# Kernel optimization log

Hardware: AMD Instinct MI355X
Metric: run time of the kernel (lower is better)

Reference implementation:

```python
import jax, jax.numpy as jnp
import numpy as np

N = 50000   # nodes
E = 800000  # raw (non-self-loop) edges
H = 4       # attention heads


def _att_coef(h, src, dst, mask, n):
    # per-edge cosine similarity (sklearn cosine_similarity gathered at edges)
    hn = h / jnp.maximum(jnp.linalg.norm(h, axis=-1, keepdims=True), 1e-12)
    sim = jnp.sum(hn[src] * hn[dst], axis=-1)              # [E]
    # threshold sim<0.1 -> 0; mask keeps only edges surviving previous layers
    sim = jnp.where(mask & (sim >= 0.1), sim, 0.0)
    # l1 row-normalization (rows indexed by src, matching adj.row)
    rowsum = jax.ops.segment_sum(sim, src, num_segments=n)
    safe = jnp.where(rowsum[src] > 0, rowsum[src], 1.0)
    att = jnp.where(rowsum[src] > 0, sim / safe, 0.0)
    new_mask = att > 0                                     # nonzero structure after threshold
    degree = jax.ops.segment_sum(new_mask.astype(h.dtype), src, num_segments=n)
    lam = 1.0 / (degree + 1.0)                             # self-loop weight per node
    att_w = jnp.where(new_mask, jnp.exp(att), 0.0)         # exp() of surviving entries
    self_w = jnp.exp(lam)
    return att_w, self_w, new_mask


def _gat_layer(h, W, a, b, src, dst, n, act):
    # DGL GATConv: W projection, additive attention, softmax over incoming edges
    HF = W.shape[1]
    F = HF // H
    feat = (h @ W).reshape(n, H, F)                        # [N,H,F]
    el = jnp.sum(feat * a[0], axis=-1)                     # [N,H]
    er = jnp.sum(feat * a[1], axis=-1)                     # [N,H]
    e = jax.nn.leaky_relu(el[src] + er[dst], 0.2)          # [Eg,H]
    emax = jax.ops.segment_max(e, dst, num_segments=n)
    ex = jnp.exp(e - emax[dst])
    z = jax.ops.segment_sum(ex, dst, num_segments=n)
    alpha = ex / z[dst]                                    # edge softmax over dst
    out = jax.ops.segment_sum(feat[src] * alpha[..., None], dst, num_segments=n)
    out = out.reshape(n, HF) + b
    return jax.nn.leaky_relu(out, 0.01) if act else out


def setup_inputs() -> dict:
    key = jax.random.key(0)
    ks = jax.random.split(key, 9)
    x = jax.random.normal(ks[0], (N, 128), jnp.float32)
    src = jax.random.randint(ks[1], (E,), 0, N, jnp.int32)
    dst = jax.random.randint(ks[2], (E,), 0, N, jnp.int32)
    dst = jnp.where(dst == src, (dst + 1) % N, dst)  # raw edges have no self-loops
    W0 = jax.random.normal(ks[3], (128, H * 64), jnp.float32) * 0.05
    a0 = jax.random.normal(ks[4], (2, H, 64), jnp.float32) * 0.05
    b0 = jnp.zeros((H * 64,), jnp.float32)
    W1 = jax.random.normal(ks[5], (H * 64, H * 64), jnp.float32) * 0.05
    a1 = jax.random.normal(ks[6], (2, H, 64), jnp.float32) * 0.05
    b1 = jnp.zeros((H * 64,), jnp.float32)
    return {"x": x, "edge_src": src, "edge_dst": dst,
            "W0": W0, "a0": a0, "b0": b0, "W1": W1, "a1": a1, "b1": b1}


def reference(x, edge_src, edge_dst, W0, a0, b0, W1, a1, b1):
    sl = jnp.arange(N, dtype=edge_src.dtype)
    src_g = jnp.concatenate([edge_src, sl])  # GATConv graph includes self-loops
    dst_g = jnp.concatenate([edge_dst, sl])
    mask = jnp.ones((E,), bool)
    # layer 0: att_coef on input features, then GATConv (+ leaky_relu activation)
    att_w, self_w, mask = _att_coef(x, edge_src, edge_dst, mask, N)
    h = _gat_layer(x, W0, a0, b0, src_g, dst_g, N, True)
    # layer 1: att_coef on hidden features (edge set shrunk by layer-0 threshold)
    att_w, self_w, mask = _att_coef(h, edge_src, edge_dst, mask, N)
    h = _gat_layer(h, W1, a1, b1, src_g, dst_g, N, False)
    return h, att_w, self_w
```

## Files before the change

### kernel.cpp

```cpp
#include <hip/hip_runtime.h>


#define NH 4
#define NF 64
#define HF 256

__device__ __forceinline__ float wred_sum(float v) {
#pragma unroll
  for (int o = 32; o > 0; o >>= 1) v += __shfl_xor(v, o, 64);
  return v;
}
__device__ __forceinline__ float lrelu(float x, float s) {
  return x > 0.f ? x : s * x;
}
__device__ __forceinline__ float bf2f(unsigned short u) {
  union { float f; unsigned int i; } v;
  v.i = ((unsigned int)u) << 16;
  return v.f;
}
__device__ __forceinline__ unsigned short f2bf(float f) {
  union { float f; unsigned int i; } v;
  v.f = f;
  unsigned int r = v.i + 0x7fffu + ((v.i >> 16) & 1u);
  return (unsigned short)(r >> 16);
}
__device__ __forceinline__ float dot_bf16x8(uint4 a, uint4 b) {
  const unsigned int* pa = (const unsigned int*)&a;
  const unsigned int* pb = (const unsigned int*)&b;
  float acc = 0.f;
#pragma unroll
  for (int i = 0; i < 4; ++i) {
    acc += bf2f((unsigned short)(pa[i] & 0xffff)) *
           bf2f((unsigned short)(pb[i] & 0xffff));
    acc += bf2f((unsigned short)(pa[i] >> 16)) *
           bf2f((unsigned short)(pb[i] >> 16));
  }
  return acc;
}
__device__ __forceinline__ float4 unpack_bf4(uint2 q) {
  return make_float4(bf2f((unsigned short)(q.x & 0xffff)),
                     bf2f((unsigned short)(q.x >> 16)),
                     bf2f((unsigned short)(q.y & 0xffff)),
                     bf2f((unsigned short)(q.y >> 16)));
}

__global__ __launch_bounds__(256) void xprep_kernel(
    const float* __restrict__ X, float* __restrict__ inv,
    unsigned short* __restrict__ xnb, int n) {
  int row = blockIdx.x * 4 + (threadIdx.x >> 6);
  int lane = threadIdx.x & 63;
  if (row >= n) return;
  float2 v = ((const float2*)(X + (size_t)row * 128))[lane];
  float acc = v.x * v.x + v.y * v.y;
  acc = wred_sum(acc);
  float s = 1.f / fmaxf(sqrtf(acc), 1e-12f);
  if (lane == 0) inv[row] = s;
  unsigned int packed =
      (unsigned int)f2bf(v.x * s) | ((unsigned int)f2bf(v.y * s) << 16);
  ((unsigned int*)(xnb + (size_t)row * 128))[lane] = packed;
}

__global__ __launch_bounds__(256) void edge_mask8_kernel(
    const unsigned short* __restrict__ xnb, const float* __restrict__ X,
    const float* __restrict__ xinv, const int* __restrict__ esrc,
    const int* __restrict__ edst, int* __restrict__ mask2, int E_) {
  int p = blockIdx.x * 32 + (threadIdx.x >> 3);
  int gl = threadIdx.x & 7;
  if (p >= E_) return;
  int s = esrc[p], d = edst[p];
  const uint4* ps = (const uint4*)(xnb + (size_t)s * 128);
  const uint4* pd = (const uint4*)(xnb + (size_t)d * 128);
  uint4 a0 = ps[gl], a1 = ps[gl + 8];
  uint4 b0 = pd[gl], b1 = pd[gl + 8];
  float acc = dot_bf16x8(a0, b0) + dot_bf16x8(a1, b1);
#pragma unroll
  for (int o = 1; o < 8; o <<= 1) acc += __shfl_xor(acc, o, 64);
  bool mk;
  if (fabsf(acc - 0.1f) < 4e-3f) {
    const float4* fs = (const float4*)(X + (size_t)s * 128);
    const float4* fd = (const float4*)(X + (size_t)d * 128);
    float a2 = 0.f;
#pragma unroll
    for (int i = 0; i < 4; ++i) {
      float4 fa = fs[gl + 8 * i], fb = fd[gl + 8 * i];
      a2 += fa.x * fb.x + fa.y * fb.y + fa.z * fb.z + fa.w * fb.w;
    }
#pragma unroll
    for (int o = 1; o < 8; o <<= 1) a2 += __shfl_xor(a2, o, 64);
    mk = (a2 * xinv[s] * xinv[d]) >= 0.1f;
  } else {
    mk = acc >= 0.1f;
  }
  if (gl == 0) mask2[p] = mk ? 1 : 0;
}

__global__ __launch_bounds__(256) void compact_kernel(
    const int* __restrict__ mask2, const int* __restrict__ pos2,
    const int* __restrict__ esrc, const int* __restrict__ edst,
    int* __restrict__ cs, int* __restrict__ cd, int* __restrict__ ce,
    int E_) {
  int p = blockIdx.x * blockDim.x + threadIdx.x;
  if (p >= E_) return;
  if (mask2[p]) {
    int q = pos2[p];
    cs[q] = esrc[p];
    cd[q] = edst[p];
    ce[q] = p;
  }
}

__global__ __launch_bounds__(256) void sim2_kernel(
    const float* __restrict__ Hf, const float* __restrict__ hinv,
    const int* __restrict__ cs, const int* __restrict__ cd,
    const int* __restrict__ total, float* __restrict__ svc,
    float* __restrict__ rowsum, float* __restrict__ degf) {
  int S = total[0];
  int gl = threadIdx.x & 15;
  int g0 = blockIdx.x * 16 + (threadIdx.x >> 4);
  int gstride = gridDim.x * 16;
  for (int q = g0; q < S; q += gstride) {
    int s = cs[q], d = cd[q];
    const float4* hs = (const float4*)(Hf + (size_t)s * 256);
    const float4* hd = (const float4*)(Hf + (size_t)d * 256);
    float acc = 0.f;
#pragma unroll
    for (int i = 0; i < 4; ++i) {
      float4 a = hs[gl + 16 * i], b = hd[gl + 16 * i];
      acc += a.x * b.x + a.y * b.y + a.z * b.z + a.w * b.w;
    }
#pragma unroll
    for (int o = 1; o < 16; o <<= 1) acc += __shfl_xor(acc, o, 64);
    if (gl == 0) {
      float sim = acc * hinv[s] * hinv[d];
      float sv = (sim >= 0.1f) ? sim : 0.f;
      svc[q] = sv;
      if (sv > 0.f) {
        atomicAdd(&rowsum[s], sv);
        atomicAdd(&degf[s], 1.0f);
      }
    }
  }
}

__global__ __launch_bounds__(256) void att_w_kernel(
    const float* __restrict__ svc, const float* __restrict__ rowsum,
    const int* __restrict__ cs, const int* __restrict__ ce,
    const int* __restrict__ total, float* __restrict__ out_att) {
  int S = total[0];
  int stride = gridDim.x * blockDim.x;
  for (int q = blockIdx.x * blockDim.x + threadIdx.x; q < S; q += stride) {
    float sv = svc[q];
    if (sv > 0.f) out_att[ce[q]] = __expf(sv / rowsum[cs[q]]);
  }
}

__global__ __launch_bounds__(256) void self_w_kernel(
    const float* __restrict__ degf, float* __restrict__ out_self, int n) {
  int i = blockIdx.x * blockDim.x + threadIdx.x;
  if (i >= n) return;
  out_self[i] = __expf(1.f / (degf[i] + 1.f));
}

__global__ __launch_bounds__(256) void gemm_kernel(
    const float* __restrict__ A, const float* __restrict__ B,
    const float* __restrict__ Av, unsigned short* __restrict__ feat16,
    float* __restrict__ el, float* __restrict__ er, int n, int K, int M) {
  __shared__ float As[16][132];
  __shared__ float Bs[16][64];
  int tid = threadIdx.x;
  int tx = tid & 15, ty = tid >> 4;
  int row0 = blockIdx.x * 128;
  int col0 = blockIdx.y * 64;
  int h = blockIdx.y;
  float acc[8][4] = {};
  for (int k0 = 0; k0 < K; k0 += 16) {
#pragma unroll
    for (int i = 0; i < 2; ++i) {
      int p = tid + i * 256;
      int r = p >> 2, c4 = p & 3;
      int gr = row0 + r;
      float4 v = make_float4(0.f, 0.f, 0.f, 0.f);
      if (gr < n) v = *(const float4*)(A + (size_t)gr * K + k0 + c4 * 4);
      As[c4 * 4 + 0][r] = v.x;
      As[c4 * 4 + 1][r] = v.y;
      As[c4 * 4 + 2][r] = v.z;
      As[c4 * 4 + 3][r] = v.w;
    }
    {
      int r = tid >> 4, c4 = tid & 15;
      *(float4*)&Bs[r][c4 * 4] =
          *(const float4*)(B + (size_t)(k0 + r) * M + col0 + c4 * 4);
    }
    __syncthreads();
#pragma unroll
    for (int k = 0; k < 16; ++k) {
      float4 a0v = *(const float4*)&As[k][ty * 4];
      float4 a1v = *(const float4*)&As[k][64 + ty * 4];
      float4 bv4 = *(const float4*)&Bs[k][tx * 4];
      float av[8] = {a0v.x, a0v.y, a0v.z, a0v.w, a1v.x, a1v.y, a1v.z, a1v.w};
      float bv[4] = {bv4.x, bv4.y, bv4.z, bv4.w};
#pragma unroll
      for (int i = 0; i < 8; ++i)
#pragma unroll
        for (int j = 0; j < 4; ++j) acc[i][j] += av[i] * bv[j];
    }
    __syncthreads();
  }
  float aEl[4], aEr[4];
#pragma unroll
  for (int j = 0; j < 4; ++j) {
    aEl[j] = Av[h * 64 + tx * 4 + j];
    aEr[j] = Av[HF + h * 64 + tx * 4 + j];
  }
#pragma unroll
  for (int half = 0; half < 2; ++half) {
#pragma unroll
    for (int i = 0; i < 4; ++i) {
      int gr = row0 + half * 64 + ty * 4 + i;
      int ai = half * 4 + i;
      float pl = 0.f, pr = 0.f;
#pragma unroll
      for (int j = 0; j < 4; ++j) {
        pl += acc[ai][j] * aEl[j];
        pr += acc[ai][j] * aEr[j];
      }
#pragma unroll
      for (int o = 1; o < 16; o <<= 1) {
        pl += __shfl_xor(pl, o, 64);
        pr += __shfl_xor(pr, o, 64);
      }
      if (gr < n) {
        unsigned int p0 = (unsigned int)f2bf(acc[ai][0]) |
                          ((unsigned int)f2bf(acc[ai][1]) << 16);
        unsigned int p1 = (unsigned int)f2bf(acc[ai][2]) |
                          ((unsigned int)f2bf(acc[ai][3]) << 16);
        ((uint2*)(feat16 + (size_t)gr * HF + col0 + tx * 4))[0] =
            make_uint2(p0, p1);
        if (tx == 0) {
          el[gr * NH + h] = pl;
          er[gr * NH + h] = pr;
        }
      }
    }
  }
}

__global__ __launch_bounds__(256) void hist_kernel(
    const int* __restrict__ key, int* __restrict__ deg, int E_) {
  int e = blockIdx.x * blockDim.x + threadIdx.x;
  if (e >= E_) return;
  atomicAdd(&deg[key[e]], 1);
}

__global__ __launch_bounds__(1024) void scanA_kernel(
    const int* __restrict__ deg, int* __restrict__ rs, int* __restrict__ bsum,
    int n) {
  __shared__ int temp[1024];
  int tid = threadIdx.x;
  int idx = blockIdx.x * 1024 + tid;
  int v = (idx < n) ? deg[idx] : 0;
  temp[tid] = v;
  __syncthreads();
  for (int off = 1; off < 1024; off <<= 1) {
    int t = (tid >= off) ? temp[tid - off] : 0;
    __syncthreads();
    temp[tid] += t;
    __syncthreads();
  }
  if (idx < n) rs[idx] = temp[tid] - v;
  if (tid == 1023) bsum[blockIdx.x] = temp[1023];
}

__global__ __launch_bounds__(1024) void scanB_kernel(int* __restrict__ bsum,
                                                     int nb) {
  __shared__ int t[1024];
  int tid = threadIdx.x;
  int v = (tid < nb) ? bsum[tid] : 0;
  t[tid] = v;
  __syncthreads();
  for (int off = 1; off < 1024; off <<= 1) {
    int u = (tid >= off) ? t[tid - off] : 0;
    __syncthreads();
    t[tid] += u;
    __syncthreads();
  }
  if (tid < nb) bsum[tid] = t[tid] - v;
  if (tid == 0) bsum[nb] = t[1023];
}

__global__ __launch_bounds__(256) void scanC_kernel(
    int* __restrict__ rs, const int* __restrict__ bsum, int n, int nb) {
  int idx = blockIdx.x * blockDim.x + threadIdx.x;
  if (idx < n) rs[idx] += bsum[idx >> 10];
  else if (idx == n) rs[n] = bsum[nb];
}

__global__ __launch_bounds__(256) void scatter_kernel(
    const int* __restrict__ src, const int* __restrict__ dst,
    const int* __restrict__ rs, int* __restrict__ cursor,
    unsigned short* __restrict__ csr_src, int E_) {
  int e = blockIdx.x * blockDim.x + threadIdx.x;
  if (e >= E_) return;
  int d = dst[e];
  int pos = rs[d] + atomicAdd(&cursor[d], 1);
  csr_src[pos] = (unsigned short)src[e];
}

__global__ __launch_bounds__(256) void gat_agg_kernel(
    const unsigned short* __restrict__ feat16, const float* __restrict__ el,
    const float* __restrict__ er, const int* __restrict__ row_start,
    const unsigned short* __restrict__ csr_src,
    const float* __restrict__ bias, float* __restrict__ out,
    float* __restrict__ inv_out, int n, int act) {
  int node = blockIdx.x * 4 + (threadIdx.x >> 6);
  int lane = threadIdx.x & 63;
  if (node >= n) return;
  int h = lane >> 4;
  const uint2* f16 = (const uint2*)feat16;
  float er_n = er[node * NH + h];
  float es = lrelu(el[node * NH + h] + er_n, 0.2f);
  int start = row_start[node];
  int deg = row_start[node + 1] - start;
  float ws = __expf(es);
  float4 fv = unpack_bf4(f16[(size_t)node * 64 + lane]);
  float4 facc = make_float4(ws * fv.x, ws * fv.y, ws * fv.z, ws * fv.w);
  float z = ws;
  for (int c = 0; c < deg; c += 8) {
    int t = c + (lane & 7);
    int myidx = (t < deg) ? (int)csr_src[start + t] : 0;
    if (deg - c >= 8) {
#pragma unroll
      for (int j = 0; j < 8; ++j) {
        int s = __shfl(myidx, j, 8);
        float w = __expf(lrelu(el[s * NH + h] + er_n, 0.2f));
        float4 f = unpack_bf4(f16[(size_t)s * 64 + lane]);
        facc.x += w * f.x;
        facc.y += w * f.y;
        facc.z += w * f.z;
        facc.w += w * f.w;
        z += w;
      }
    } else {
      int m8 = deg - c;
      for (int j = 0; j < m8; ++j) {
        int s = __shfl(myidx, j, 8);
        float w = __expf(lrelu(el[s * NH + h] + er_n, 0.2f));
        float4 f = unpack_bf4(f16[(size_t)s * 64 + lane]);
        facc.x += w * f.x;
        facc.y += w * f.y;
        facc.z += w * f.z;
        facc.w += w * f.w;
        z += w;
      }
    }
  }
  float rz = 1.f / z;
  float4 bb = ((const float4*)bias)[lane];
  float4 o_;
  o_.x = facc.x * rz + bb.x;
  o_.y = facc.y * rz + bb.y;
  o_.z = facc.z * rz + bb.z;
  o_.w = facc.w * rz + bb.w;
  if (act) {
    o_.x = lrelu(o_.x, 0.01f);
    o_.y = lrelu(o_.y, 0.01f);
    o_.z = lrelu(o_.z, 0.01f);
    o_.w = lrelu(o_.w, 0.01f);
  }
  ((float4*)out)[(size_t)node * 64 + lane] = o_;
  if (inv_out) {
    float sq = o_.x * o_.x + o_.y * o_.y + o_.z * o_.z + o_.w * o_.w;
    sq = wred_sum(sq);
    if (lane == 0) inv_out[node] = 1.f / fmaxf(sqrtf(sq), 1e-12f);
  }
}

extern "C" void kernel_launch(void* const* d_in, const int* in_sizes, int n_in,
                              void* d_out, int out_size, void* d_ws, size_t ws_size,
                              hipStream_t stream) {
  const float* x = (const float*)d_in[0];
  const int* esrc = (const int*)d_in[1];
  const int* edst = (const int*)d_in[2];
  const float* W0 = (const float*)d_in[3];
  const float* a0 = (const float*)d_in[4];
  const float* b0 = (const float*)d_in[5];
  const float* W1 = (const float*)d_in[6];
  const float* a1 = (const float*)d_in[7];
  const float* b1 = (const float*)d_in[8];

  const int N = in_sizes[0] / 128;
  const int E = in_sizes[1];

  char* wp = (char*)d_ws;
  auto alloc = [&](size_t bytes) {
    char* p = wp;
    wp += (bytes + 255) & ~(size_t)255;
    return p;
  };
  float* h0 = (float*)alloc((size_t)N * HF * 4);
  unsigned short* feat16 = (unsigned short*)alloc((size_t)N * HF * 2);
  unsigned short* xnb = (unsigned short*)alloc((size_t)N * 128 * 2);
  float* xinv = (float*)alloc((size_t)N * 4);
  float* h0inv = (float*)alloc((size_t)N * 4);
  float* el = (float*)alloc((size_t)N * NH * 4);
  float* er = (float*)alloc((size_t)N * NH * 4);
  float* svc = (float*)alloc((size_t)E * 4);
  int* row_start = (int*)alloc((size_t)(N + 1) * 4);
  unsigned short* csr_src = (unsigned short*)alloc((size_t)E * 2);
  int* cs = (int*)alloc((size_t)E * 4);
  int* cd = (int*)alloc((size_t)E * 4);
  int* ce = (int*)alloc((size_t)E * 4);
  int* mask2 = (int*)alloc((size_t)E * 4);
  int* pos2 = (int*)alloc((size_t)(E + 1) * 4);
  const int NSB = (N + 1023) / 1024;
  const int ESB = (E + 1023) / 1024;
  int* bsum = (int*)alloc((size_t)(NSB + 1) * 4);
  int* bsumE = (int*)alloc((size_t)(ESB + 1) * 4);
  char* zero_base = wp;
  int* deg_i = (int*)alloc((size_t)N * 4);
  int* cursor = (int*)alloc((size_t)N * 4);
  float* rowsum = (float*)alloc((size_t)N * 4);
  float* degf = (float*)alloc((size_t)N * 4);
  size_t zero_bytes = (size_t)(wp - zero_base);

  float* out_h = (float*)d_out;
  float* out_att = out_h + (size_t)N * HF;
  float* out_self = out_att + E;

  const int NB4 = (N + 3) / 4;
  const int EBT = (E + 255) / 256;
  const int NBT = (N + 255) / 256;
  const int EB8 = (E + 31) / 32;

  hipMemsetAsync(zero_base, 0, zero_bytes, stream);
  hipMemsetAsync(out_att, 0, (size_t)E * 4, stream);

  hist_kernel<<<EBT, 256, 0, stream>>>(edst, deg_i, E);
  scanA_kernel<<<NSB, 1024, 0, stream>>>(deg_i, row_start, bsum, N);
  scanB_kernel<<<1, 1024, 0, stream>>>(bsum, NSB);
  scanC_kernel<<<(N + 256) / 256, 256, 0, stream>>>(row_start, bsum, N, NSB);
  scatter_kernel<<<EBT, 256, 0, stream>>>(esrc, edst, row_start, cursor,
                                          csr_src, E);

  xprep_kernel<<<NB4, 256, 0, stream>>>(x, xinv, xnb, N);
  edge_mask8_kernel<<<EB8, 256, 0, stream>>>(xnb, x, xinv, esrc, edst, mask2,
                                             E);
  scanA_kernel<<<ESB, 1024, 0, stream>>>(mask2, pos2, bsumE, E);
  scanB_kernel<<<1, 1024, 0, stream>>>(bsumE, ESB);
  scanC_kernel<<<(E + 256) / 256, 256, 0, stream>>>(pos2, bsumE, E, ESB);
  compact_kernel<<<EBT, 256, 0, stream>>>(mask2, pos2, esrc, edst, cs, cd, ce,
                                          E);

  {
    dim3 g((N + 127) / 128, HF / 64);
    gemm_kernel<<<g, 256, 0, stream>>>(x, W0, a0, feat16, el, er, N, 128, HF);
  }
  gat_agg_kernel<<<NB4, 256, 0, stream>>>(feat16, el, er, row_start, csr_src,
                                          b0, h0, h0inv, N, 1);

  sim2_kernel<<<1024, 256, 0, stream>>>(h0, h0inv, cs, cd, pos2 + E, svc,
                                        rowsum, degf);
  att_w_kernel<<<512, 256, 0, stream>>>(svc, rowsum, cs, ce, pos2 + E,
                                        out_att);
  self_w_kernel<<<NBT, 256, 0, stream>>>(degf, out_self, N);

  {
    dim3 g((N + 127) / 128, HF / 64);
    gemm_kernel<<<g, 256, 0, stream>>>(h0, W1, a1, feat16, el, er, N, 256, HF);
  }
  gat_agg_kernel<<<NB4, 256, 0, stream>>>(feat16, el, er, row_start, csr_src,
                                          b1, out_h, nullptr, N, 0);
}
```

Measured before the change: 584.9 us.

## Replace FP32 SIMT GEMMs with FP16 MFMA GEMMs using pre-packed weights

Replaces the shared-memory FP32 tiled GEMM with an MFMA 16x16x32 f16 kernel. Inputs are converted to fp16 by the existing prep and aggregation kernels, and weights are repacked into a per-lane fragment layout by a new kernel. This aims to cut the FMA-bound projection cost for both layers, at the price of fp16 input precision, extra fp16 copies of the activations, and scattered 2-byte feature stores in the epilogue.

```diff
diff --git a/kernel.cpp b/kernel.cpp
--- a/kernel.cpp
+++ b/kernel.cpp
@@ -4,6 +4,10 @@
 #define NH 4
 #define NF 64
 #define HF 256
+
+typedef _Float16 f16x8 __attribute__((ext_vector_type(8)));
+typedef _Float16 f16x4 __attribute__((ext_vector_type(4)));
+typedef float f32x4 __attribute__((ext_vector_type(4)));
 
 __device__ __forceinline__ float wred_sum(float v) {
 #pragma unroll
@@ -46,7 +50,7 @@
 
 __global__ __launch_bounds__(256) void xprep_kernel(
     const float* __restrict__ X, float* __restrict__ inv,
-    unsigned short* __restrict__ xnb, int n) {
+    unsigned short* __restrict__ xnb, _Float16* __restrict__ x16, int n) {
   int row = blockIdx.x * 4 + (threadIdx.x >> 6);
   int lane = threadIdx.x & 63;
   if (row >= n) return;
@@ -58,6 +62,9 @@
   unsigned int packed =
       (unsigned int)f2bf(v.x * s) | ((unsigned int)f2bf(v.y * s) << 16);
   ((unsigned int*)(xnb + (size_t)row * 128))[lane] = packed;
+  _Float16 h0v = (_Float16)v.x, h1v = (_Float16)v.y;
+  x16[(size_t)row * 128 + 2 * lane] = h0v;
+  x16[(size_t)row * 128 + 2 * lane + 1] = h1v;
 }
 
 __global__ __launch_bounds__(256) void edge_mask8_kernel(
@@ -161,84 +168,82 @@
   out_self[i] = __expf(1.f / (degf[i] + 1.f));
 }
 
-__global__ __launch_bounds__(256) void gemm_kernel(
-    const float* __restrict__ A, const float* __restrict__ B,
+__global__ __launch_bounds__(256) void wpack_kernel(
+    const float* __restrict__ W, _Float16* __restrict__ Wf, int K) {
+  int KC = K >> 5;
+  int u = blockIdx.x * 256 + threadIdx.x;
+  int total = 16 * KC * 64;
+  if (u >= total) return;
+  int l = u & 63;
+  int kc = (u >> 6) % KC;
+  int htc = (u >> 6) / KC;
+  int col = (htc >> 2) * 64 + (htc & 3) * 16 + (l & 15);
+  int kb = kc * 32 + (l >> 4) * 8;
+  f16x8 o;
+#pragma unroll
+  for (int j = 0; j < 8; ++j) o[j] = (_Float16)W[(size_t)(kb + j) * HF + col];
+  *(f16x8*)(Wf + (size_t)u * 8) = o;
+}
+
+__global__ __launch_bounds__(256) void gemm_mfma_kernel(
+    const _Float16* __restrict__ A16, const _Float16* __restrict__ Wf,
     const float* __restrict__ Av, unsigned short* __restrict__ feat16,
-    float* __restrict__ el, float* __restrict__ er, int n, int K, int M) {
-  __shared__ float As[16][132];
-  __shared__ float Bs[16][64];
-  int tid = threadIdx.x;
-  int tx = tid & 15, ty = tid >> 4;
-  int row0 = blockIdx.x * 128;
-  int col0 = blockIdx.y * 64;
+    float* __restrict__ el, float* __restrict__ er, int n, int K) {
+  int wave = threadIdx.x >> 6;
+  int lane = threadIdx.x & 63;
   int h = blockIdx.y;
-  float acc[8][4] = {};
-  for (int k0 = 0; k0 < K; k0 += 16) {
-#pragma unroll
-    for (int i = 0; i < 2; ++i) {
-      int p = tid + i * 256;
-      int r = p >> 2, c4 = p & 3;
-      int gr = row0 + r;
-      float4 v = make_float4(0.f, 0.f, 0.f, 0.f);
-      if (gr < n) v = *(const float4*)(A + (size_t)gr * K + k0 + c4 * 4);
-      As[c4 * 4 + 0][r] = v.x;
-      As[c4 * 4 + 1][r] = v.y;
-      As[c4 * 4 + 2][r] = v.z;
-      As[c4 * 4 + 3][r] = v.w;
-    }
-    {
-      int r = tid >> 4, c4 = tid & 15;
-      *(float4*)&Bs[r][c4 * 4] =
-          *(const float4*)(B + (size_t)(k0 + r) * M + col0 + c4 * 4);
-    }
-    __syncthreads();
-#pragma unroll
-    for (int k = 0; k < 16; ++k) {
-      float4 a0v = *(const float4*)&As[k][ty * 4];
-      float4 a1v = *(const float4*)&As[k][64 + ty * 4];
-      float4 bv4 = *(const float4*)&Bs[k][tx * 4];
-      float av[8] = {a0v.x, a0v.y, a0v.z, a0v.w, a1v.x, a1v.y, a1v.z, a1v.w};
-      float bv[4] = {bv4.x, bv4.y, bv4.z, bv4.w};
-#pragma unroll
-      for (int i = 0; i < 8; ++i)
-#pragma unroll
-        for (int j = 0; j < 4; ++j) acc[i][j] += av[i] * bv[j];
-    }
-    __syncthreads();
+  int row0 = blockIdx.x * 128 + wave * 32;
+  int KC = K >> 5;
+  int rA = lane & 15, gk = lane >> 4;
+  f32x4 acc[2][4] = {};
+  const _Float16* a0p =
+      A16 + (size_t)min(row0 + rA, n - 1) * K + gk * 8;
+  const _Float16* a1p =
+      A16 + (size_t)min(row0 + 16 + rA, n - 1) * K + gk * 8;
+  const f16x8* bf = (const f16x8*)(Wf + (size_t)h * 4 * KC * 512);
+  for (int kc = 0; kc < KC; ++kc) {
+    f16x8 af0 = *(const f16x8*)(a0p + kc * 32);
+    f16x8 af1 = *(const f16x8*)(a1p + kc * 32);
+#pragma unroll
+    for (int tc = 0; tc < 4; ++tc) {
+      f16x8 bfr = bf[(tc * KC + kc) * 64 + lane];
+      acc[0][tc] =
+          __builtin_amdgcn_mfma_f32_16x16x32_f16(af0, bfr, acc[0][tc], 0, 0, 0);
+      acc[1][tc] =
+          __builtin_amdgcn_mfma_f32_16x16x32_f16(af1, bfr, acc[1][tc], 0, 0, 0);
+    }
   }
   float aEl[4], aEr[4];
 #pragma unroll
-  for (int j = 0; j < 4; ++j) {
-    aEl[j] = Av[h * 64 + tx * 4 + j];
-    aEr[j] = Av[HF + h * 64 + tx * 4 + j];
-  }
-#pragma unroll
-  for (int half = 0; half < 2; ++half) {
-#pragma unroll
-    for (int i = 0; i < 4; ++i) {
-      int gr = row0 + half * 64 + ty * 4 + i;
-      int ai = half * 4 + i;
+  for (int tc = 0; tc < 4; ++tc) {
+    aEl[tc] = Av[h * 64 + tc * 16 + rA];
+    aEr[tc] = Av[HF + h * 64 + tc * 16 + rA];
+  }
+#pragma unroll
+  for (int tr = 0; tr < 2; ++tr) {
+#pragma unroll
+    for (int r = 0; r < 4; ++r) {
+      int row = row0 + tr * 16 + gk * 4 + r;
       float pl = 0.f, pr = 0.f;
 #pragma unroll
-      for (int j = 0; j < 4; ++j) {
-        pl += acc[ai][j] * aEl[j];
-        pr += acc[ai][j] * aEr[j];
+      for (int tc = 0; tc < 4; ++tc) {
+        float v = acc[tr][tc][r];
+        pl += v * aEl[tc];
+        pr += v * aEr[tc];
       }
 #pragma unroll
       for (int o = 1; o < 16; o <<= 1) {
         pl += __shfl_xor(pl, o, 64);
         pr += __shfl_xor(pr, o, 64);
       }
-      if (gr < n) {
-        unsigned int p0 = (unsigned int)f2bf(acc[ai][0]) |
-                          ((unsigned int)f2bf(acc[ai][1]) << 16);
-        unsigned int p1 = (unsigned int)f2bf(acc[ai][2]) |
-                          ((unsigned int)f2bf(acc[ai][3]) << 16);
-        ((uint2*)(feat16 + (size_t)gr * HF + col0 + tx * 4))[0] =
-            make_uint2(p0, p1);
-        if (tx == 0) {
-          el[gr * NH + h] = pl;
-          er[gr * NH + h] = pr;
+      if (row < n) {
+#pragma unroll
+        for (int tc = 0; tc < 4; ++tc)
+          feat16[(size_t)row * HF + h * 64 + tc * 16 + rA] =
+              f2bf(acc[tr][tc][r]);
+        if (rA == 0) {
+          el[row * NH + h] = pl;
+          er[row * NH + h] = pr;
         }
       }
     }
@@ -311,7 +316,8 @@
     const float* __restrict__ er, const int* __restrict__ row_start,
     const unsigned short* __restrict__ csr_src,
     const float* __restrict__ bias, float* __restrict__ out,
-    float* __restrict__ inv_out, int n, int act) {
+    float* __restrict__ inv_out, _Float16* __restrict__ h016, int n,
+    int act) {
   int node = blockIdx.x * 4 + (threadIdx.x >> 6);
   int lane = threadIdx.x & 63;
   if (node >= n) return;
@@ -369,6 +375,12 @@
   }
   ((float4*)out)[(size_t)node * 64 + lane] = o_;
   if (inv_out) {
+    f16x4 hv;
+    hv[0] = (_Float16)o_.x;
+    hv[1] = (_Float16)o_.y;
+    hv[2] = (_Float16)o_.z;
+    hv[3] = (_Float16)o_.w;
+    *(f16x4*)(h016 + (size_t)node * HF + lane * 4) = hv;
     float sq = o_.x * o_.x + o_.y * o_.y + o_.z * o_.z + o_.w * o_.w;
     sq = wred_sum(sq);
     if (lane == 0) inv_out[node] = 1.f / fmaxf(sqrtf(sq), 1e-12f);
@@ -400,6 +412,10 @@
   float* h0 = (float*)alloc((size_t)N * HF * 4);
   unsigned short* feat16 = (unsigned short*)alloc((size_t)N * HF * 2);
   unsigned short* xnb = (unsigned short*)alloc((size_t)N * 128 * 2);
+  _Float16* x16 = (_Float16*)alloc((size_t)N * 128 * 2);
+  _Float16* h016 = (_Float16*)alloc((size_t)N * HF * 2);
+  _Float16* Wf0 = (_Float16*)alloc((size_t)128 * HF * 2);
+  _Float16* Wf1 = (_Float16*)alloc((size_t)256 * HF * 2);
   float* xinv = (float*)alloc((size_t)N * 4);
   float* h0inv = (float*)alloc((size_t)N * 4);
   float* el = (float*)alloc((size_t)N * NH * 4);
@@ -442,7 +458,10 @@
   scatter_kernel<<<EBT, 256, 0, stream>>>(esrc, edst, row_start, cursor,
                                           csr_src, E);
 
-  xprep_kernel<<<NB4, 256, 0, stream>>>(x, xinv, xnb, N);
+  wpack_kernel<<<(16 * 4 * 64 + 255) / 256, 256, 0, stream>>>(W0, Wf0, 128);
+  wpack_kernel<<<(16 * 8 * 64 + 255) / 256, 256, 0, stream>>>(W1, Wf1, 256);
+
+  xprep_kernel<<<NB4, 256, 0, stream>>>(x, xinv, xnb, x16, N);
   edge_mask8_kernel<<<EB8, 256, 0, stream>>>(xnb, x, xinv, esrc, edst, mask2,
                                              E);
   scanA_kernel<<<ESB, 1024, 0, stream>>>(mask2, pos2, bsumE, E);
@@ -452,11 +471,12 @@
                                           E);
 
   {
-    dim3 g((N + 127) / 128, HF / 64);
-    gemm_kernel<<<g, 256, 0, stream>>>(x, W0, a0, feat16, el, er, N, 128, HF);
+    dim3 g((N + 127) / 128, NH);
+    gemm_mfma_kernel<<<g, 256, 0, stream>>>(x16, Wf0, a0, feat16, el, er, N,
+                                            128);
   }
   gat_agg_kernel<<<NB4, 256, 0, stream>>>(feat16, el, er, row_start, csr_src,
-                                          b0, h0, h0inv, N, 1);
+                                          b0, h0, h0inv, h016, N, 1);
 
   sim2_kernel<<<1024, 256, 0, stream>>>(h0, h0inv, cs, cd, pos2 + E, svc,
                                         rowsum, degf);
@@ -465,9 +485,10 @@
   self_w_kernel<<<NBT, 256, 0, stream>>>(degf, out_self, N);
 
   {
-    dim3 g((N + 127) / 128, HF / 64);
-    gemm_kernel<<<g, 256, 0, stream>>>(h0, W1, a1, feat16, el, er, N, 256, HF);
+    dim3 g((N + 127) / 128, NH);
+    gemm_mfma_kernel<<<g, 256, 0, stream>>>(h016, Wf1, a1, feat16, el, er, N,
+                                            256);
   }
   gat_agg_kernel<<<NB4, 256, 0, stream>>>(feat16, el, er, row_start, csr_src,
-                                          b1, out_h, nullptr, N, 0);
-}
+                                          b1, out_h, nullptr, nullptr, N, 0);
+}
```

After: 491.2 us. 1.19x faster.
